# Kernel optimization log

Measured on AMD Instinct MI355X. Metric: run time of the kernel, lower is better.

The kernel has to match this reference:

```python
import jax, jax.numpy as jnp
import numpy as np

N_NODES = 100000

def setup_inputs() -> dict:
    key = jax.random.key(0)
    k1, k2, k3, k4, k5 = jax.random.split(key, 5)
    E = 1600000
    feat = jax.random.normal(k1, (N_NODES, 128), dtype=jnp.float32)
    W = jax.random.normal(k2, (128, 32), dtype=jnp.float32) * 0.08  # ~xavier scale
    edge_w = jax.random.uniform(k3, (E,), dtype=jnp.float32)
    src = jax.random.randint(k4, (E,), 0, N_NODES, dtype=jnp.int32)
    dst = jax.random.randint(k5, (E,), 0, N_NODES, dtype=jnp.int32)
    return {"feat": feat, "W": W, "edge_w": edge_w, "src": src, "dst": dst}

def reference(feat, W, edge_w, src, dst):
    # linear transform: [N, in] @ [in, out] -> [N, out]
    h = feat @ W
    # gather source features per edge, scale by edge weight: u_mul_e
    m = h[src] * edge_w[:, None]  # [E, out]
    # sum messages at destination nodes
    rst = jax.ops.segment_sum(m, dst, num_segments=N_NODES)  # [N, out]
    return rst
```

## Files before the change

kernel.cpp:

```cpp
#include <hip/hip_runtime.h>
#include <hip/hip_fp16.h>

constexpr int N_IN    = 128;
constexpr int N_OUT   = 32;
constexpr int LOG_R   = 6;
constexpr int RANGE   = 1 << LOG_R;
constexpr int MAXNB   = 2048;
constexpr int NCC     = 256;
constexpr int FBLK    = 512;
constexpr int CHUNK_P = 2048;

union H4 { uint2 u; __half2 h2[2]; };
union H8 { uint4 u; __half2 h2[4]; };

__global__ __launch_bounds__(FBLK) void gemm_part_k(
    const float* __restrict__ feat, const float* __restrict__ W,
    const int* __restrict__ src, const int* __restrict__ dst,
    const float* __restrict__ ew, __half* __restrict__ h,
    int* __restrict__ tbl, int2* __restrict__ sw,
    int n, int E, int NB, int epc, int ncc)
{
    __shared__ __align__(16) char smem[N_IN * N_OUT * sizeof(float)];
    const int tid = threadIdx.x;

    if ((int)blockIdx.x < ncc) {
        int* hist  = (int*)smem;
        int* wscan = (int*)(smem + MAXNB * 4);

        const int c   = blockIdx.x;
        const int e0  = c * epc;
        const int e1  = min(e0 + epc, E);
        const int m   = max(e1 - e0, 0);
        const int m4  = m & ~3;
        const int slots = (NB + FBLK - 1) / FBLK;

        for (int i = tid; i < NB; i += FBLK) hist[i] = 0;
        __syncthreads();

        for (int o = tid * 4; o < m4; o += FBLK * 4) {
            int4 dv = *reinterpret_cast<const int4*>(dst + e0 + o);
            atomicAdd(&hist[dv.x >> LOG_R], 1);
            atomicAdd(&hist[dv.y >> LOG_R], 1);
            atomicAdd(&hist[dv.z >> LOG_R], 1);
            atomicAdd(&hist[dv.w >> LOG_R], 1);
        }
        if (m4 + tid < m) atomicAdd(&hist[dst[e0 + m4 + tid] >> LOG_R], 1);
        __syncthreads();

        int tsum = 0;
        int base = tid * slots;
        for (int j = 0; j < slots; ++j) {
            int idx = base + j;
            if (idx < NB) tsum += hist[idx];
        }
        wscan[tid] = tsum;
        __syncthreads();
        for (int off = 1; off < FBLK; off <<= 1) {
            int x = (tid >= off) ? wscan[tid - off] : 0;
            __syncthreads();
            wscan[tid] += x;
            __syncthreads();
        }
        int run = wscan[tid] - tsum;
        __syncthreads();
        for (int j = 0; j < slots; ++j) {
            int idx = base + j;
            if (idx < NB) {
                int cval = hist[idx];
                tbl[(size_t)c * (NB + 1) + idx] = run;
                hist[idx] = run;
                run += cval;
            }
        }
        if (tid == 0) tbl[(size_t)c * (NB + 1) + NB] = m;
        __syncthreads();

        int2* outp = sw + (size_t)c * epc;
        for (int o = tid * 4; o < m4; o += FBLK * 4) {
            int4   sv = *reinterpret_cast<const int4*>(src + e0 + o);
            int4   dv = *reinterpret_cast<const int4*>(dst + e0 + o);
            float4 wv = *reinterpret_cast<const float4*>(ew + e0 + o);
            int p0 = atomicAdd(&hist[dv.x >> LOG_R], 1);
            int p1 = atomicAdd(&hist[dv.y >> LOG_R], 1);
            int p2 = atomicAdd(&hist[dv.z >> LOG_R], 1);
            int p3 = atomicAdd(&hist[dv.w >> LOG_R], 1);
            outp[p0] = make_int2(sv.x | ((dv.x & (RANGE - 1)) << 17), __float_as_int(wv.x));
            outp[p1] = make_int2(sv.y | ((dv.y & (RANGE - 1)) << 17), __float_as_int(wv.y));
            outp[p2] = make_int2(sv.z | ((dv.z & (RANGE - 1)) << 17), __float_as_int(wv.z));
            outp[p3] = make_int2(sv.w | ((dv.w & (RANGE - 1)) << 17), __float_as_int(wv.w));
        }
        if (m4 + tid < m) {
            int e = e0 + m4 + tid;
            int d = dst[e];
            int pos = atomicAdd(&hist[d >> LOG_R], 1);
            outp[pos] = make_int2(src[e] | ((d & (RANGE - 1)) << 17), __float_as_int(ew[e]));
        }
    } else {
        float* Ws = (float*)smem;
        for (int i = tid; i < (N_IN * N_OUT) / 4; i += FBLK)
            reinterpret_cast<float4*>(Ws)[i] = reinterpret_cast<const float4*>(W)[i];
        __syncthreads();

        int gid = ((int)blockIdx.x - ncc) * FBLK + tid;
        int row = gid >> 3;
        if (row >= n) return;
        int cg = (gid & 7) * 4;

        const float4* frow = reinterpret_cast<const float4*>(feat + (size_t)row * N_IN);
        float4 acc = make_float4(0.f, 0.f, 0.f, 0.f);
        #pragma unroll
        for (int k4 = 0; k4 < N_IN / 4; ++k4) {
            float4 f = frow[k4];
            int k = k4 * 4;
            float4 w0 = *reinterpret_cast<const float4*>(&Ws[(k + 0) * N_OUT + cg]);
            float4 w1 = *reinterpret_cast<const float4*>(&Ws[(k + 1) * N_OUT + cg]);
            float4 w2 = *reinterpret_cast<const float4*>(&Ws[(k + 2) * N_OUT + cg]);
            float4 w3 = *reinterpret_cast<const float4*>(&Ws[(k + 3) * N_OUT + cg]);
            acc.x += f.x * w0.x + f.y * w1.x + f.z * w2.x + f.w * w3.x;
            acc.y += f.x * w0.y + f.y * w1.y + f.z * w2.y + f.w * w3.y;
            acc.z += f.x * w0.z + f.y * w1.z + f.z * w2.z + f.w * w3.z;
            acc.w += f.x * w0.w + f.y * w1.w + f.z * w2.w + f.w * w3.w;
        }
        H4 v;
        v.h2[0] = __float22half2_rn(make_float2(acc.x, acc.y));
        v.h2[1] = __float22half2_rn(make_float2(acc.z, acc.w));
        *reinterpret_cast<uint2*>(h + (size_t)row * N_OUT + cg) = v.u;
    }
}

__global__ __launch_bounds__(256) void conv6_k(
    const __half* __restrict__ h, const int2* __restrict__ sw,
    const int* __restrict__ tbl, float* __restrict__ out,
    int n, int NB, int ncc, int epc)
{
    __shared__ int2 pairs[CHUNK_P];
    __shared__ unsigned short order[CHUNK_P];
    __shared__ int cnt[RANGE];
    __shared__ int sc[RANGE];
    __shared__ int start[RANGE + 1];
    __shared__ int cur[RANGE];
    __shared__ int rs[NCC];
    __shared__ int ps[NCC + 1];
    __shared__ int stmp[256];

    const int b    = blockIdx.x;
    const int tid  = threadIdx.x;
    const int node = tid >> 2;
    const int cg8  = (tid & 3) * 8;

    int len = 0;
    if (tid < ncc) {
        int s0 = tbl[(size_t)tid * (NB + 1) + b];
        int s1 = tbl[(size_t)tid * (NB + 1) + b + 1];
        rs[tid] = s0;
        len = s1 - s0;
    }
    stmp[tid] = len;
    __syncthreads();
    for (int off = 1; off < 256; off <<= 1) {
        int x = (tid >= off) ? stmp[tid - off] : 0;
        __syncthreads();
        stmp[tid] += x;
        __syncthreads();
    }
    ps[tid + 1] = stmp[tid];
    if (tid == 0) ps[0] = 0;
    __syncthreads();
    const int deg = ps[ncc];

    float4 acc01 = make_float4(0.f, 0.f, 0.f, 0.f);
    float4 acc23 = make_float4(0.f, 0.f, 0.f, 0.f);

    #define GLOAD(p, f0, f1, f2, f3)                                           \
        H8 _x##f0;                                                             \
        _x##f0.u = *reinterpret_cast<const uint4*>(                            \
            h + (size_t)((p).x & 0x1FFFF) * N_OUT + cg8);                      \
        float2 f0 = __half22float2(_x##f0.h2[0]);                              \
        float2 f1 = __half22float2(_x##f0.h2[1]);                              \
        float2 f2 = __half22float2(_x##f0.h2[2]);                              \
        float2 f3 = __half22float2(_x##f0.h2[3]);
    #define GACC(p, f0, f1, f2, f3)                                            \
    {                                                                          \
        float wv = __int_as_float((p).y);                                      \
        acc01.x += f0.x * wv; acc01.y += f0.y * wv;                            \
        acc01.z += f1.x * wv; acc01.w += f1.y * wv;                            \
        acc23.x += f2.x * wv; acc23.y += f2.y * wv;                            \
        acc23.z += f3.x * wv; acc23.w += f3.y * wv;                            \
    }

    if (deg <= CHUNK_P) {
        if (tid < RANGE) cnt[tid] = 0;
        __syncthreads();

        {
            int d0 = ps[tid];
            int l  = ps[tid + 1] - d0;
            const int2* sp = sw + (size_t)tid * epc + rs[tid];
            for (int j = 0; j < l; ++j) {
                int2 p = sp[j];
                pairs[d0 + j] = p;
                atomicAdd(&cnt[p.x >> 17], 1);
            }
        }
        __syncthreads();

        int v = 0;
        if (tid < RANGE) { v = cnt[tid]; sc[tid] = v; }
        __syncthreads();
        #pragma unroll
        for (int off = 1; off < RANGE; off <<= 1) {
            int x = (tid < RANGE && tid >= off) ? sc[tid - off] : 0;
            __syncthreads();
            if (tid < RANGE) sc[tid] += x;
            __syncthreads();
        }
        if (tid < RANGE) { start[tid] = sc[tid] - v; cur[tid] = sc[tid] - v; }
        if (tid == RANGE - 1) start[RANGE] = sc[RANGE - 1];
        __syncthreads();

        for (int i = tid; i < deg; i += 256) {
            int loc = pairs[i].x >> 17;
            int pos = atomicAdd(&cur[loc], 1);
            order[pos] = (unsigned short)i;
        }
        __syncthreads();

        int k  = start[node];
        int ke = start[node + 1];
        for (; k + 7 < ke; k += 8) {
            int2 q0 = pairs[order[k + 0]], q1 = pairs[order[k + 1]];
            int2 q2 = pairs[order[k + 2]], q3 = pairs[order[k + 3]];
            int2 q4 = pairs[order[k + 4]], q5 = pairs[order[k + 5]];
            int2 q6 = pairs[order[k + 6]], q7 = pairs[order[k + 7]];
            GLOAD(q0, m0, m1, m2, m3)
            GLOAD(q1, n0, n1, n2, n3)
            GLOAD(q2, o0, o1, o2, o3)
            GLOAD(q3, p0, p1, p2, p3)
            GLOAD(q4, r0, r1, r2, r3)
            GLOAD(q5, s0, s1, s2, s3)
            GLOAD(q6, t0, t1, t2, t3)
            GLOAD(q7, u0, u1, u2, u3)
            GACC(q0, m0, m1, m2, m3)
            GACC(q1, n0, n1, n2, n3)
            GACC(q2, o0, o1, o2, o3)
            GACC(q3, p0, p1, p2, p3)
            GACC(q4, r0, r1, r2, r3)
            GACC(q5, s0, s1, s2, s3)
            GACC(q6, t0, t1, t2, t3)
            GACC(q7, u0, u1, u2, u3)
        }
        for (; k + 3 < ke; k += 4) {
            int2 q0 = pairs[order[k + 0]], q1 = pairs[order[k + 1]];
            int2 q2 = pairs[order[k + 2]], q3 = pairs[order[k + 3]];
            GLOAD(q0, a0, a1, a2, a3)
            GLOAD(q1, b0, b1, b2, b3)
            GLOAD(q2, c0, c1, c2, c3)
            GLOAD(q3, d0, d1, d2, d3)
            GACC(q0, a0, a1, a2, a3)
            GACC(q1, b0, b1, b2, b3)
            GACC(q2, c0, c1, c2, c3)
            GACC(q3, d0, d1, d2, d3)
        }
        for (; k < ke; ++k) {
            int2 q = pairs[order[k]];
            GLOAD(q, e0, e1, e2, e3)
            GACC(q, e0, e1, e2, e3)
        }
    } else {
        for (int cbase = 0; cbase < deg; cbase += CHUNK_P) {
            const int m = min(CHUNK_P, deg - cbase);
            for (int i = tid; i < m; i += 256) {
                int gidx = cbase + i;
                int lo = 0, hi = ncc - 1;
                while (lo < hi) {
                    int mid = (lo + hi + 1) >> 1;
                    if (ps[mid] <= gidx) lo = mid; else hi = mid - 1;
                }
                int off = gidx - ps[lo];
                pairs[i] = sw[(size_t)lo * epc + rs[lo] + off];
            }
            __syncthreads();
            for (int k = 0; k < m; ++k) {
                int2 p = pairs[k];
                if ((p.x >> 17) == node) {
                    GLOAD(p, f0, f1, f2, f3)
                    GACC(p, f0, f1, f2, f3)
                }
            }
            __syncthreads();
        }
    }
    #undef GLOAD
    #undef GACC

    int node0 = b * RANGE + node;
    if (node0 < n) {
        float* o = out + (size_t)node0 * N_OUT + cg8;
        *reinterpret_cast<float4*>(o + 0) = acc01;
        *reinterpret_cast<float4*>(o + 4) = acc23;
    }
}

__global__ __launch_bounds__(256) void fused_edge(
    const float* __restrict__ feat, const float* __restrict__ W,
    const float* __restrict__ edge_w, const int* __restrict__ src,
    const int* __restrict__ dst, float* __restrict__ out, int E)
{
    __shared__ float Ws[N_IN * N_OUT];
    for (int i = threadIdx.x; i < (N_IN * N_OUT) / 4; i += 256)
        reinterpret_cast<float4*>(Ws)[i] = reinterpret_cast<const float4*>(W)[i];
    __syncthreads();
    int gid = blockIdx.x * 256 + threadIdx.x;
    int e = gid >> 3;
    if (e >= E) return;
    int cg = (gid & 7) * 4;
    int s = src[e];
    int d = dst[e];
    float w = edge_w[e];
    const float4* frow = reinterpret_cast<const float4*>(feat + (size_t)s * N_IN);
    float4 acc = make_float4(0.f, 0.f, 0.f, 0.f);
    #pragma unroll
    for (int k4 = 0; k4 < N_IN / 4; ++k4) {
        float4 f = frow[k4];
        int k = k4 * 4;
        float4 w0 = *reinterpret_cast<const float4*>(&Ws[(k + 0) * N_OUT + cg]);
        float4 w1 = *reinterpret_cast<const float4*>(&Ws[(k + 1) * N_OUT + cg]);
        float4 w2 = *reinterpret_cast<const float4*>(&Ws[(k + 2) * N_OUT + cg]);
        float4 w3 = *reinterpret_cast<const float4*>(&Ws[(k + 3) * N_OUT + cg]);
        acc.x += f.x * w0.x + f.y * w1.x + f.z * w2.x + f.w * w3.x;
        acc.y += f.x * w0.y + f.y * w1.y + f.z * w2.y + f.w * w3.y;
        acc.z += f.x * w0.z + f.y * w1.z + f.z * w2.z + f.w * w3.z;
        acc.w += f.x * w0.w + f.y * w1.w + f.z * w2.w + f.w * w3.w;
    }
    float* o = out + (size_t)d * N_OUT + cg;
    atomicAdd(o + 0, acc.x * w);
    atomicAdd(o + 1, acc.y * w);
    atomicAdd(o + 2, acc.z * w);
    atomicAdd(o + 3, acc.w * w);
}

extern "C" void kernel_launch(void* const* d_in, const int* in_sizes, int n_in,
                              void* d_out, int out_size, void* d_ws, size_t ws_size,
                              hipStream_t stream) {
    const float* feat   = (const float*)d_in[0];
    const float* W      = (const float*)d_in[1];
    const float* edge_w = (const float*)d_in[2];
    const int*   src    = (const int*)d_in[3];
    const int*   dst    = (const int*)d_in[4];
    float* out = (float*)d_out;

    int n = in_sizes[0] / N_IN;
    int E = in_sizes[2];

    int NB  = (n + RANGE - 1) / RANGE;
    int ncc = NCC;
    int epc = (((E + ncc - 1) / ncc) + 3) & ~3;

    size_t off_h   = 0;
    size_t off_tbl = (off_h + (size_t)n * N_OUT * sizeof(__half) + 15) & ~(size_t)15;
    size_t off_sw  = (off_tbl + (size_t)ncc * (NB + 1) * sizeof(int) + 15) & ~(size_t)15;
    size_t need    = off_sw + (size_t)ncc * epc * sizeof(int2);

    bool ok = (ws_size >= need) && (n <= (1 << 17)) && (NB <= MAXNB);

    if (ok) {
        char* ws = (char*)d_ws;
        __half* h  = (__half*)(ws + off_h);
        int*   tbl = (int*)(ws + off_tbl);
        int2*  sw  = (int2*)(ws + off_sw);

        int gemm_blocks = (int)(((long)n * 8 + FBLK - 1) / FBLK);
        gemm_part_k<<<ncc + gemm_blocks, FBLK, 0, stream>>>(
            feat, W, src, dst, edge_w, h, tbl, sw, n, E, NB, epc, ncc);
        conv6_k<<<NB, 256, 0, stream>>>(h, sw, tbl, out, n, NB, ncc, epc);
    } else {
        hipError_t _e = hipMemsetAsync(d_out, 0, (size_t)out_size * sizeof(float), stream);
        (void)_e;
        long sthreads = (long)E * 8;
        fused_edge<<<(int)((sthreads + 255) / 256), 256, 0, stream>>>(feat, W, edge_w, src, dst, out, E);
    }
}
```

Measured before the change: 71.71 us.

## Split fused GEMM/partition kernel into separate GEMM and partition launches

The single kernel that ran edge partitioning blocks alongside GEMM blocks is split into two kernels launched back to back on the same stream. The GEMM now uses 256-thread blocks, and the partition kernel has its own statically sized shared memory. This simplifies each kernel's resource usage (LDS, block size), which may raise occupancy. The cost is an extra launch and the loss of concurrent execution of the GEMM and partition work.

```diff
diff --git a/kernel.cpp b/kernel.cpp
--- a/kernel.cpp
+++ b/kernel.cpp
@@ -7,124 +7,123 @@
 constexpr int RANGE   = 1 << LOG_R;
 constexpr int MAXNB   = 2048;
 constexpr int NCC     = 256;
-constexpr int FBLK    = 512;
+constexpr int PBLK    = 512;
 constexpr int CHUNK_P = 2048;
 
 union H4 { uint2 u; __half2 h2[2]; };
 union H8 { uint4 u; __half2 h2[4]; };
 
-__global__ __launch_bounds__(FBLK) void gemm_part_k(
+__global__ __launch_bounds__(256) void gemm_h(
     const float* __restrict__ feat, const float* __restrict__ W,
+    __half* __restrict__ h, int n)
+{
+    __shared__ float Ws[N_IN * N_OUT];
+    for (int i = threadIdx.x; i < (N_IN * N_OUT) / 4; i += 256)
+        reinterpret_cast<float4*>(Ws)[i] = reinterpret_cast<const float4*>(W)[i];
+    __syncthreads();
+
+    int gid = blockIdx.x * 256 + threadIdx.x;
+    int row = gid >> 3;
+    if (row >= n) return;
+    int cg = (gid & 7) * 4;
+
+    const float4* frow = reinterpret_cast<const float4*>(feat + (size_t)row * N_IN);
+    float4 acc = make_float4(0.f, 0.f, 0.f, 0.f);
+    #pragma unroll
+    for (int k4 = 0; k4 < N_IN / 4; ++k4) {
+        float4 f = frow[k4];
+        int k = k4 * 4;
+        float4 w0 = *reinterpret_cast<const float4*>(&Ws[(k + 0) * N_OUT + cg]);
+        float4 w1 = *reinterpret_cast<const float4*>(&Ws[(k + 1) * N_OUT + cg]);
+        float4 w2 = *reinterpret_cast<const float4*>(&Ws[(k + 2) * N_OUT + cg]);
+        float4 w3 = *reinterpret_cast<const float4*>(&Ws[(k + 3) * N_OUT + cg]);
+        acc.x += f.x * w0.x + f.y * w1.x + f.z * w2.x + f.w * w3.x;
+        acc.y += f.x * w0.y + f.y * w1.y + f.z * w2.y + f.w * w3.y;
+        acc.z += f.x * w0.z + f.y * w1.z + f.z * w2.z + f.w * w3.z;
+        acc.w += f.x * w0.w + f.y * w1.w + f.z * w2.w + f.w * w3.w;
+    }
+    H4 v;
+    v.h2[0] = __float22half2_rn(make_float2(acc.x, acc.y));
+    v.h2[1] = __float22half2_rn(make_float2(acc.z, acc.w));
+    *reinterpret_cast<uint2*>(h + (size_t)row * N_OUT + cg) = v.u;
+}
+
+__global__ __launch_bounds__(PBLK) void partition2_k(
     const int* __restrict__ src, const int* __restrict__ dst,
-    const float* __restrict__ ew, __half* __restrict__ h,
-    int* __restrict__ tbl, int2* __restrict__ sw,
-    int n, int E, int NB, int epc, int ncc)
+    const float* __restrict__ w, int* __restrict__ tbl,
+    int2* __restrict__ sw, int E, int NB, int epc)
 {
-    __shared__ __align__(16) char smem[N_IN * N_OUT * sizeof(float)];
+    __shared__ int hist[MAXNB];
+    __shared__ int wscan[PBLK];
+
+    const int c   = blockIdx.x;
     const int tid = threadIdx.x;
-
-    if ((int)blockIdx.x < ncc) {
-        int* hist  = (int*)smem;
-        int* wscan = (int*)(smem + MAXNB * 4);
-
-        const int c   = blockIdx.x;
-        const int e0  = c * epc;
-        const int e1  = min(e0 + epc, E);
-        const int m   = max(e1 - e0, 0);
-        const int m4  = m & ~3;
-        const int slots = (NB + FBLK - 1) / FBLK;
-
-        for (int i = tid; i < NB; i += FBLK) hist[i] = 0;
-        __syncthreads();
-
-        for (int o = tid * 4; o < m4; o += FBLK * 4) {
-            int4 dv = *reinterpret_cast<const int4*>(dst + e0 + o);
-            atomicAdd(&hist[dv.x >> LOG_R], 1);
-            atomicAdd(&hist[dv.y >> LOG_R], 1);
-            atomicAdd(&hist[dv.z >> LOG_R], 1);
-            atomicAdd(&hist[dv.w >> LOG_R], 1);
-        }
-        if (m4 + tid < m) atomicAdd(&hist[dst[e0 + m4 + tid] >> LOG_R], 1);
-        __syncthreads();
-
-        int tsum = 0;
-        int base = tid * slots;
-        for (int j = 0; j < slots; ++j) {
-            int idx = base + j;
-            if (idx < NB) tsum += hist[idx];
-        }
-        wscan[tid] = tsum;
-        __syncthreads();
-        for (int off = 1; off < FBLK; off <<= 1) {
-            int x = (tid >= off) ? wscan[tid - off] : 0;
-            __syncthreads();
-            wscan[tid] += x;
-            __syncthreads();
-        }
-        int run = wscan[tid] - tsum;
-        __syncthreads();
-        for (int j = 0; j < slots; ++j) {
-            int idx = base + j;
-            if (idx < NB) {
-                int cval = hist[idx];
-                tbl[(size_t)c * (NB + 1) + idx] = run;
-                hist[idx] = run;
-                run += cval;
-            }
-        }
-        if (tid == 0) tbl[(size_t)c * (NB + 1) + NB] = m;
-        __syncthreads();
-
-        int2* outp = sw + (size_t)c * epc;
-        for (int o = tid * 4; o < m4; o += FBLK * 4) {
-            int4   sv = *reinterpret_cast<const int4*>(src + e0 + o);
-            int4   dv = *reinterpret_cast<const int4*>(dst + e0 + o);
-            float4 wv = *reinterpret_cast<const float4*>(ew + e0 + o);
-            int p0 = atomicAdd(&hist[dv.x >> LOG_R], 1);
-            int p1 = atomicAdd(&hist[dv.y >> LOG_R], 1);
-            int p2 = atomicAdd(&hist[dv.z >> LOG_R], 1);
-            int p3 = atomicAdd(&hist[dv.w >> LOG_R], 1);
-            outp[p0] = make_int2(sv.x | ((dv.x & (RANGE - 1)) << 17), __float_as_int(wv.x));
-            outp[p1] = make_int2(sv.y | ((dv.y & (RANGE - 1)) << 17), __float_as_int(wv.y));
-            outp[p2] = make_int2(sv.z | ((dv.z & (RANGE - 1)) << 17), __float_as_int(wv.z));
-            outp[p3] = make_int2(sv.w | ((dv.w & (RANGE - 1)) << 17), __float_as_int(wv.w));
-        }
-        if (m4 + tid < m) {
-            int e = e0 + m4 + tid;
-            int d = dst[e];
-            int pos = atomicAdd(&hist[d >> LOG_R], 1);
-            outp[pos] = make_int2(src[e] | ((d & (RANGE - 1)) << 17), __float_as_int(ew[e]));
-        }
-    } else {
-        float* Ws = (float*)smem;
-        for (int i = tid; i < (N_IN * N_OUT) / 4; i += FBLK)
-            reinterpret_cast<float4*>(Ws)[i] = reinterpret_cast<const float4*>(W)[i];
-        __syncthreads();
-
-        int gid = ((int)blockIdx.x - ncc) * FBLK + tid;
-        int row = gid >> 3;
-        if (row >= n) return;
-        int cg = (gid & 7) * 4;
-
-        const float4* frow = reinterpret_cast<const float4*>(feat + (size_t)row * N_IN);
-        float4 acc = make_float4(0.f, 0.f, 0.f, 0.f);
-        #pragma unroll
-        for (int k4 = 0; k4 < N_IN / 4; ++k4) {
-            float4 f = frow[k4];
-            int k = k4 * 4;
-            float4 w0 = *reinterpret_cast<const float4*>(&Ws[(k + 0) * N_OUT + cg]);
-            float4 w1 = *reinterpret_cast<const float4*>(&Ws[(k + 1) * N_OUT + cg]);
-            float4 w2 = *reinterpret_cast<const float4*>(&Ws[(k + 2) * N_OUT + cg]);
-            float4 w3 = *reinterpret_cast<const float4*>(&Ws[(k + 3) * N_OUT + cg]);
-            acc.x += f.x * w0.x + f.y * w1.x + f.z * w2.x + f.w * w3.x;
-            acc.y += f.x * w0.y + f.y * w1.y + f.z * w2.y + f.w * w3.y;
-            acc.z += f.x * w0.z + f.y * w1.z + f.z * w2.z + f.w * w3.z;
-            acc.w += f.x * w0.w + f.y * w1.w + f.z * w2.w + f.w * w3.w;
-        }
-        H4 v;
-        v.h2[0] = __float22half2_rn(make_float2(acc.x, acc.y));
-        v.h2[1] = __float22half2_rn(make_float2(acc.z, acc.w));
-        *reinterpret_cast<uint2*>(h + (size_t)row * N_OUT + cg) = v.u;
+    const int e0  = c * epc;
+    const int e1  = min(e0 + epc, E);
+    const int m   = max(e1 - e0, 0);
+    const int m4  = m & ~3;
+    const int slots = (NB + PBLK - 1) / PBLK;
+
+    for (int i = tid; i < NB; i += PBLK) hist[i] = 0;
+    __syncthreads();
+
+    for (int o = tid * 4; o < m4; o += PBLK * 4) {
+        int4 dv = *reinterpret_cast<const int4*>(dst + e0 + o);
+        atomicAdd(&hist[dv.x >> LOG_R], 1);
+        atomicAdd(&hist[dv.y >> LOG_R], 1);
+        atomicAdd(&hist[dv.z >> LOG_R], 1);
+        atomicAdd(&hist[dv.w >> LOG_R], 1);
+    }
+    if (m4 + tid < m) atomicAdd(&hist[dst[e0 + m4 + tid] >> LOG_R], 1);
+    __syncthreads();
+
+    int tsum = 0;
+    int base = tid * slots;
+    for (int j = 0; j < slots; ++j) {
+        int idx = base + j;
+        if (idx < NB) tsum += hist[idx];
+    }
+    wscan[tid] = tsum;
+    __syncthreads();
+    for (int off = 1; off < PBLK; off <<= 1) {
+        int x = (tid >= off) ? wscan[tid - off] : 0;
+        __syncthreads();
+        wscan[tid] += x;
+        __syncthreads();
+    }
+    int run = wscan[tid] - tsum;
+    __syncthreads();
+    for (int j = 0; j < slots; ++j) {
+        int idx = base + j;
+        if (idx < NB) {
+            int cval = hist[idx];
+            tbl[(size_t)c * (NB + 1) + idx] = run;
+            hist[idx] = run;
+            run += cval;
+        }
+    }
+    if (tid == 0) tbl[(size_t)c * (NB + 1) + NB] = m;
+    __syncthreads();
+
+    int2* outp = sw + (size_t)c * epc;
+    for (int o = tid * 4; o < m4; o += PBLK * 4) {
+        int4   sv = *reinterpret_cast<const int4*>(src + e0 + o);
+        int4   dv = *reinterpret_cast<const int4*>(dst + e0 + o);
+        float4 wv = *reinterpret_cast<const float4*>(w + e0 + o);
+        int p0 = atomicAdd(&hist[dv.x >> LOG_R], 1);
+        int p1 = atomicAdd(&hist[dv.y >> LOG_R], 1);
+        int p2 = atomicAdd(&hist[dv.z >> LOG_R], 1);
+        int p3 = atomicAdd(&hist[dv.w >> LOG_R], 1);
+        outp[p0] = make_int2(sv.x | ((dv.x & (RANGE - 1)) << 17), __float_as_int(wv.x));
+        outp[p1] = make_int2(sv.y | ((dv.y & (RANGE - 1)) << 17), __float_as_int(wv.y));
+        outp[p2] = make_int2(sv.z | ((dv.z & (RANGE - 1)) << 17), __float_as_int(wv.z));
+        outp[p3] = make_int2(sv.w | ((dv.w & (RANGE - 1)) << 17), __float_as_int(wv.w));
+    }
+    if (m4 + tid < m) {
+        int e = e0 + m4 + tid;
+        int d = dst[e];
+        int pos = atomicAdd(&hist[d >> LOG_R], 1);
+        outp[pos] = make_int2(src[e] | ((d & (RANGE - 1)) << 17), __float_as_int(w[e]));
     }
 }
 
@@ -369,9 +368,9 @@
         int*   tbl = (int*)(ws + off_tbl);
         int2*  sw  = (int2*)(ws + off_sw);
 
-        int gemm_blocks = (int)(((long)n * 8 + FBLK - 1) / FBLK);
-        gemm_part_k<<<ncc + gemm_blocks, FBLK, 0, stream>>>(
-            feat, W, src, dst, edge_w, h, tbl, sw, n, E, NB, epc, ncc);
+        long gthreads = (long)n * 8;
+        gemm_h<<<(int)((gthreads + 255) / 256), 256, 0, stream>>>(feat, W, h, n);
+        partition2_k<<<ncc, PBLK, 0, stream>>>(src, dst, edge_w, tbl, sw, E, NB, epc);
         conv6_k<<<NB, 256, 0, stream>>>(h, sw, tbl, out, n, NB, ncc, epc);
     } else {
         hipError_t _e = hipMemsetAsync(d_out, 0, (size_t)out_size * sizeof(float), stream);
```

After: 75.82 us. 5.7% more time.
